# Kernel optimization log

Hardware: AMD Instinct MI355X
Metric: run time of the kernel (lower is better)

The kernel has to match this reference:

```python
import jax, jax.numpy as jnp
import numpy as np

HEADS = 16
DIM_HEAD = 64
SOFTCAP = 50.0
ROPE_THETA = 10000.0


def setup_inputs() -> dict:
    key = jax.random.key(0)
    ks = jax.random.split(key, 5)
    b, n, d, m, lmax = 2, 2048, 1024, 4, 256
    x = jax.random.normal(ks[0], (b, n, d), dtype=jnp.float32)
    tokens = jax.random.normal(ks[1], (b, m, lmax, d), dtype=jnp.float32)
    offsets = jnp.array([100, 600, 1100, 1600], dtype=jnp.int64)
    modalities = jnp.stack(
        [jnp.zeros_like(offsets), offsets, jnp.full_like(offsets, lmax)], axis=-1
    )  # [m, 3] = (type, offset, length)
    modalities = jnp.broadcast_to(modalities, (b, m, 3))
    gamma = jax.random.normal(ks[2], (d,), dtype=jnp.float32) * 0.02
    w_qkv = jax.random.normal(ks[3], (d, 3 * HEADS * DIM_HEAD), dtype=jnp.float32) / np.sqrt(d)
    w_out = jax.random.normal(ks[4], (HEADS * DIM_HEAD, d), dtype=jnp.float32) / np.sqrt(d)
    return {"x": x, "tokens": tokens, "gamma": gamma, "w_qkv": w_qkv,
            "w_out": w_out, "modalities": modalities}


def _apply_rotary(t, pos):
    # t: [b h n dh], pos: [b n] integer rotary positions (interleaved-pair rotation)
    freqs = 1.0 / (ROPE_THETA ** (jnp.arange(0, DIM_HEAD, 2, dtype=jnp.float32) / DIM_HEAD))
    ang = pos[:, None, :, None].astype(jnp.float32) * freqs  # [b 1 n dh/2]
    cos, sin = jnp.cos(ang), jnp.sin(ang)
    t1, t2 = t[..., ::2], t[..., 1::2]
    out = jnp.stack([t1 * cos - t2 * sin, t1 * sin + t2 * cos], axis=-1)
    return out.reshape(t.shape)


def reference(x, tokens, gamma, w_qkv, w_out, modalities):
    b, n, d = x.shape
    lmax = tokens.shape[2]
    off = modalities[..., 1]   # [b m]
    ln = modalities[..., 2]    # [b m]
    seq = jnp.arange(n)

    # --- embed_modality_tokens: scatter modality tokens into sequence ---
    in_span = (seq[None, None, :] >= off[..., None]) & (seq[None, None, :] < (off + ln)[..., None])  # [b m n]
    is_any = in_span.any(axis=1)  # [b n]
    rel = jnp.clip(seq[None, None, :] - off[..., None], 0, lmax - 1)  # [b m n]
    gathered = jnp.take_along_axis(tokens, rel[..., None], axis=2)  # [b m n d]
    mod_embed = jnp.einsum('bmn,bmnd->bnd', in_span.astype(x.dtype), gathered)
    x = jnp.where(is_any[..., None], mod_embed, x)

    # --- derive_rotary_positions_from_modality_positions (offset=[+1,-1]) ---
    rot_span = (seq[None, None, :] >= (off + 1)[..., None]) & (seq[None, None, :] < (off + ln)[..., None])
    pos = seq[None, :] - jnp.cumsum(rot_span.any(axis=1).astype(jnp.int32), axis=-1)  # [b n]

    # --- naive_attn_mask: causal OR within-modality bidirectional ---
    causal = seq[:, None] >= seq[None, :]  # [i j]
    mod_mask = ((seq[None, None, :, None] >= off[..., None, None]) &
                (seq[None, None, None, :] < (off + ln)[..., None, None])).any(axis=1)  # [b i j]
    mask = causal[None] | mod_mask  # [b i j]

    # --- Attention ---
    scale = DIM_HEAD ** -0.5
    xn = x / jnp.clip(jnp.linalg.norm(x, axis=-1, keepdims=True), 1e-12)
    xn = xn * (d ** 0.5) * (gamma + 1.0)  # RMSNorm (l2norm * sqrt(dim) * (gamma+1))
    qkv = (xn @ w_qkv).reshape(b, n, 3, HEADS, DIM_HEAD)
    q, k, v = (jnp.transpose(qkv[:, :, i], (0, 2, 1, 3)) for i in range(3))  # [b h n dh]
    q = _apply_rotary(q, pos)
    k = _apply_rotary(k, pos)
    scores = jnp.einsum('bhid,bhjd->bhij', q, k) * scale
    scores = jnp.tanh(scores / SOFTCAP) * SOFTCAP  # softclamp
    scores = jnp.where(mask[:, None], scores, -jnp.inf)
    attn = jax.nn.softmax(scores, axis=-1)
    out = jnp.einsum('bhij,bhjd->bhid', attn, v)
    out = jnp.transpose(out, (0, 2, 1, 3)).reshape(b, n, HEADS * DIM_HEAD)
    return out @ w_out
```

## Files before the change

kernel.cpp:

```cpp
#include <hip/hip_runtime.h>
#include <stdint.h>

#define HH 16
#define DHD 64
#define BB 2
#define NN 2048
#define DD 1024
#define MMOD 4
#define LMAX 256
#define BNROWS (BB*NN)
#define QKVN (3*HH*DHD)

typedef __attribute__((ext_vector_type(4))) float f32x4;
typedef __attribute__((ext_vector_type(8))) short s16x8;
typedef __attribute__((ext_vector_type(4))) short s16x4;

__device__ __forceinline__ float bf2f(unsigned short b) {
  return __uint_as_float(((unsigned int)b) << 16);
}
__device__ __forceinline__ unsigned short f2bf(float f) {
  unsigned int u = __float_as_uint(f);
  u += 0x7fffu + ((u >> 16) & 1u);
  return (unsigned short)(u >> 16);
}
__device__ __forceinline__ unsigned int cvt_pk_bf16(float a, float b) {
  unsigned int r;
  asm("v_cvt_pk_bf16_f32 %0, %1, %2" : "=v"(r) : "v"(a), "v"(b));
  return r;
}

#define ASYNC_LDS16(g, l) \
  __builtin_amdgcn_global_load_lds((const __attribute__((address_space(1))) void*)(g), \
                                   (__attribute__((address_space(3))) void*)(l), 16, 0, 0)

__global__ __launch_bounds__(256) void k_prep(const float* __restrict__ x,
                                              const float* __restrict__ tokens,
                                              const float* __restrict__ gamma,
                                              const int* __restrict__ mods,
                                              unsigned short* __restrict__ xn) {
  int bs = blockIdx.x;
  int bb = bs / NN, s = bs % NN;
  int t = threadIdx.x;
  int c = t * 4;
  const float4 xv = *(const float4*)(x + (size_t)bs * DD + c);
  float4 acc = {0.f, 0.f, 0.f, 0.f};
  bool any = false;
  #pragma unroll
  for (int m = 0; m < MMOD; ++m) {
    int off = mods[(bb * MMOD + m) * 3 + 1];
    int ln  = mods[(bb * MMOD + m) * 3 + 2];
    if (s >= off && s < off + ln) {
      any = true;
      int rel = s - off;
      if (rel > LMAX - 1) rel = LMAX - 1;
      if (rel < 0) rel = 0;
      const float4 tv = *(const float4*)(tokens + ((size_t)(bb * MMOD + m) * LMAX + rel) * DD + c);
      acc.x += tv.x; acc.y += tv.y; acc.z += tv.z; acc.w += tv.w;
    }
  }
  float4 v = any ? acc : xv;
  float ss = v.x*v.x + v.y*v.y + v.z*v.z + v.w*v.w;
  #pragma unroll
  for (int o = 32; o; o >>= 1) ss += __shfl_xor(ss, o);
  __shared__ float red[4];
  int wv = t >> 6;
  if ((t & 63) == 0) red[wv] = ss;
  __syncthreads();
  float tot = red[0] + red[1] + red[2] + red[3];
  float norm = sqrtf(tot);
  norm = fmaxf(norm, 1e-12f);
  float sc = 32.0f / norm;
  const float4 g = *(const float4*)(gamma + c);
  unsigned long long pk =
      (unsigned long long)f2bf(v.x * sc * (g.x + 1.f)) |
      ((unsigned long long)f2bf(v.y * sc * (g.y + 1.f)) << 16) |
      ((unsigned long long)f2bf(v.z * sc * (g.z + 1.f)) << 32) |
      ((unsigned long long)f2bf(v.w * sc * (g.w + 1.f)) << 48);
  *(unsigned long long*)(xn + (size_t)bs * DD + c) = pk;
}

__global__ void k_pos(const int* __restrict__ mods, int* __restrict__ pos) {
  int bb = blockIdx.x;
  int lane = threadIdx.x;
  int offs[MMOD], ends[MMOD];
  #pragma unroll
  for (int m = 0; m < MMOD; ++m) {
    int off = mods[(bb * MMOD + m) * 3 + 1];
    int ln  = mods[(bb * MMOD + m) * 3 + 2];
    offs[m] = off + 1;
    ends[m] = off + ln;
  }
  int base = lane * (NN / 64);
  int lc[NN / 64];
  int tot = 0;
  #pragma unroll
  for (int i = 0; i < NN / 64; ++i) {
    int s = base + i;
    int f = 0;
    #pragma unroll
    for (int m = 0; m < MMOD; ++m)
      if (s >= offs[m] && s < ends[m]) f = 1;
    tot += f;
    lc[i] = tot;
  }
  int v = tot;
  #pragma unroll
  for (int o = 1; o < 64; o <<= 1) {
    int u = __shfl_up(v, o);
    if (lane >= o) v += u;
  }
  int excl = v - tot;
  #pragma unroll
  for (int i = 0; i < NN / 64; ++i)
    pos[bb * NN + base + i] = base + i - (excl + lc[i]);
}

__global__ void k_tab(const int* __restrict__ pos, float2* __restrict__ tab) {
  int gid = blockIdx.x * 256 + threadIdx.x;
  int p = gid & 31;
  int bs = gid >> 5;
  float inv = expf(-((float)p / 32.f) * 9.210340371976184f);
  float ang = (float)pos[bs] * inv;
  float sn, cs;
  sincosf(ang, &sn, &cs);
  tab[gid] = make_float2(cs, sn);
}

__global__ void k_tr(const float* __restrict__ in, unsigned short* __restrict__ out,
                     int R, int C) {
  __shared__ float tile[32][33];
  int bx = blockIdx.x, by = blockIdx.y;
  int tx = threadIdx.x, ty = threadIdx.y;
  #pragma unroll
  for (int k = 0; k < 4; ++k) {
    int r = by * 32 + ty + k * 8, c = bx * 32 + tx;
    tile[ty + k * 8][tx] = in[(size_t)r * C + c];
  }
  __syncthreads();
  #pragma unroll
  for (int k = 0; k < 4; ++k) {
    int oc = bx * 32 + ty + k * 8;
    int orr = by * 32 + tx;
    out[(size_t)oc * R + orr] = f2bf(tile[tx][ty + k * 8]);
  }
}

template<bool F32OUT>
__global__ __launch_bounds__(256) void k_gemm(const unsigned short* __restrict__ A,
                                              const unsigned short* __restrict__ Bt,
                                              void* __restrict__ Cp,
                                              int M, int Nn, int K) {
  __shared__ unsigned short As[2][128 * 64];
  __shared__ unsigned short Bs[2][128 * 64];
  int tid = threadIdx.x;
  int lane = tid & 63, wv = tid >> 6;
  int lo = lane & 15, hi = lane >> 4;
  int nb = gridDim.x * gridDim.y;
  int fid = blockIdx.y * gridDim.x + blockIdx.x;
  int cpx = nb >> 3;
  int nid = (fid & 7) * cpx + (fid >> 3);
  int m0 = (nid / gridDim.x) * 128;
  int n0 = (nid % gridDim.x) * 128;
  int wr = wv >> 1, wc = wv & 1;
  f32x4 acc[4][4] = {};

  int srow = tid >> 3;
  int scs  = ((tid & 7) ^ ((tid >> 3) & 7)) * 8;
  #define STAGE_G(BUF, KT) do { \
    _Pragma("unroll") \
    for (int is_ = 0; is_ < 4; ++is_) { \
      int r_ = is_ * 32 + srow; \
      const unsigned short* ga_ = A  + (size_t)(m0 + r_) * K + (KT) + scs; \
      const unsigned short* gb_ = Bt + (size_t)(n0 + r_) * K + (KT) + scs; \
      ASYNC_LDS16(ga_, &As[BUF][(is_ * 256 + wv * 64) * 8]); \
      ASYNC_LDS16(gb_, &Bs[BUF][(is_ * 256 + wv * 64) * 8]); \
    } \
  } while (0)

  int nt = K >> 6;
  STAGE_G(0, 0);
  __syncthreads();
  int buf = 0;
  for (int t = 0; t < nt; ++t) {
    if (t + 1 < nt) STAGE_G(buf ^ 1, (t + 1) << 6);
    #pragma unroll
    for (int ks = 0; ks < 2; ++ks) {
      s16x8 af[4], bfr[4];
      #pragma unroll
      for (int m = 0; m < 4; ++m) {
        int row = wr * 64 + m * 16 + lo;
        int cc = ((ks * 4 + hi) ^ (lo & 7)) * 8;
        af[m] = *(const s16x8*)&As[buf][row * 64 + cc];
      }
      #pragma unroll
      for (int nn = 0; nn < 4; ++nn) {
        int row = wc * 64 + nn * 16 + lo;
        int cc = ((ks * 4 + hi) ^ (lo & 7)) * 8;
        bfr[nn] = *(const s16x8*)&Bs[buf][row * 64 + cc];
      }
      #pragma unroll
      for (int m = 0; m < 4; ++m)
        #pragma unroll
        for (int nn = 0; nn < 4; ++nn)
          acc[m][nn] = __builtin_amdgcn_mfma_f32_16x16x32_bf16(af[m], bfr[nn], acc[m][nn], 0, 0, 0);
    }
    __syncthreads();
    buf ^= 1;
  }
  #undef STAGE_G

  #pragma unroll
  for (int m = 0; m < 4; ++m) {
    #pragma unroll
    for (int nn = 0; nn < 4; ++nn) {
      int r0 = m0 + wr * 64 + m * 16 + hi * 4;
      int cc = n0 + wc * 64 + nn * 16 + lo;
      #pragma unroll
      for (int j = 0; j < 4; ++j) {
        float val = acc[m][nn][j];
        if (F32OUT) ((float*)Cp)[(size_t)(r0 + j) * Nn + cc] = val;
        else        ((unsigned short*)Cp)[(size_t)(r0 + j) * Nn + cc] = f2bf(val);
      }
    }
  }
}

__global__ __launch_bounds__(256) void k_gemm_n64(const unsigned short* __restrict__ A,
                                                  const unsigned short* __restrict__ Bt,
                                                  float* __restrict__ C,
                                                  int M, int Nn, int K) {
  __shared__ unsigned short As[2][128 * 64];
  __shared__ unsigned short Bs[2][64 * 64];
  int tid = threadIdx.x;
  int lane = tid & 63, wv = tid >> 6;
  int lo = lane & 15, hi = lane >> 4;
  int nb = gridDim.x * gridDim.y;
  int fid = blockIdx.y * gridDim.x + blockIdx.x;
  int cpx = nb >> 3;
  int nid = (fid & 7) * cpx + (fid >> 3);
  int m0 = (nid / gridDim.x) * 128;
  int n0 = (nid % gridDim.x) * 64;
  f32x4 acc[2][4] = {};

  int srow = tid >> 3;
  int scs  = ((tid & 7) ^ ((tid >> 3) & 7)) * 8;
  #define STAGE_N(BUF, KT) do { \
    _Pragma("unroll") \
    for (int is_ = 0; is_ < 4; ++is_) { \
      int r_ = is_ * 32 + srow; \
      const unsigned short* ga_ = A + (size_t)(m0 + r_) * K + (KT) + scs; \
      ASYNC_LDS16(ga_, &As[BUF][(is_ * 256 + wv * 64) * 8]); \
    } \
    _Pragma("unroll") \
    for (int is_ = 0; is_ < 2; ++is_) { \
      int r_ = is_ * 32 + srow; \
      const unsigned short* gb_ = Bt + (size_t)(n0 + r_) * K + (KT) + scs; \
      ASYNC_LDS16(gb_, &Bs[BUF][(is_ * 256 + wv * 64) * 8]); \
    } \
  } while (0)

  int nt = K >> 6;
  STAGE_N(0, 0);
  __syncthreads();
  int buf = 0;
  for (int t = 0; t < nt; ++t) {
    if (t + 1 < nt) STAGE_N(buf ^ 1, (t + 1) << 6);
    #pragma unroll
    for (int ks = 0; ks < 2; ++ks) {
      s16x8 af[2], bfr[4];
      #pragma unroll
      for (int m = 0; m < 2; ++m) {
        int row = wv * 32 + m * 16 + lo;
        int cc = ((ks * 4 + hi) ^ (lo & 7)) * 8;
        af[m] = *(const s16x8*)&As[buf][row * 64 + cc];
      }
      #pragma unroll
      for (int nn = 0; nn < 4; ++nn) {
        int row = nn * 16 + lo;
        int cc = ((ks * 4 + hi) ^ (lo & 7)) * 8;
        bfr[nn] = *(const s16x8*)&Bs[buf][row * 64 + cc];
      }
      #pragma unroll
      for (int m = 0; m < 2; ++m)
        #pragma unroll
        for (int nn = 0; nn < 4; ++nn)
          acc[m][nn] = __builtin_amdgcn_mfma_f32_16x16x32_bf16(af[m], bfr[nn], acc[m][nn], 0, 0, 0);
    }
    __syncthreads();
    buf ^= 1;
  }
  #undef STAGE_N

  #pragma unroll
  for (int m = 0; m < 2; ++m)
    #pragma unroll
    for (int nn = 0; nn < 4; ++nn) {
      int r0 = m0 + wv * 32 + m * 16 + hi * 4;
      int cc = n0 + nn * 16 + lo;
      #pragma unroll
      for (int j = 0; j < 4; ++j)
        C[(size_t)(r0 + j) * Nn + cc] = acc[m][nn][j];
    }
}

__global__ __launch_bounds__(256) void k_rope(const unsigned short* __restrict__ qkv,
                                              const float2* __restrict__ tab,
                                              unsigned short* __restrict__ k) {
  int bs = blockIdx.x;
  int bb = bs / NN, s = bs % NN;
  int lane = threadIdx.x & 63, wv = threadIdx.x >> 6;
  #pragma unroll
  for (int g = 16 + wv; g < 32; g += 4) {
    int h = g & 15;
    float val = bf2f(qkv[(size_t)bs * QKVN + g * 64 + lane]);
    float partner = __shfl_xor(val, 1);
    float2 cs = tab[(size_t)bs * 32 + (lane >> 1)];
    float out;
    if ((lane & 1) == 0) out = val * cs.x - partner * cs.y;
    else                 out = partner * cs.y + val * cs.x;
    k[((size_t)(bb * HH + h) * NN + s) * 64 + lane] = f2bf(out);
  }
}

__global__ __launch_bounds__(256) void k_vtr(const unsigned short* __restrict__ qkvt,
                                             unsigned short* __restrict__ vT) {
  __shared__ unsigned short t[64][72];
  int s0 = blockIdx.x * 64, bh = blockIdx.y, bb = bh >> 4, h = bh & 15;
  int tid = threadIdx.x;
  int r = tid >> 2, c0 = (tid & 3) * 16;
  int cw = c0 ^ (((r >> 4) & 3) << 4);
  const unsigned short* src = qkvt + (size_t)(bb * NN + s0 + r) * QKVN + 2048 + h * 64 + c0;
  *(s16x8*)&t[r][cw]     = *(const s16x8*)src;
  *(s16x8*)&t[r][cw + 8] = *(const s16x8*)(src + 8);
  __syncthreads();
  int dh = tid >> 2, sc = (tid & 3) * 16;
  int col2 = dh ^ ((tid & 3) << 4);
  s16x8 o1, o2;
  #pragma unroll
  for (int i = 0; i < 8; ++i) {
    o1[i] = (short)t[sc + i][col2];
    o2[i] = (short)t[sc + 8 + i][col2];
  }
  unsigned short* dst = vT + ((size_t)bh * 64 + dh) * NN + s0;
  int pb = (sc & 32) + (((sc >> 4) & 1) << 2);
  s16x4 g0 = __builtin_shufflevector(o1, o1, 0, 1, 2, 3);
  s16x4 g1 = __builtin_shufflevector(o1, o1, 4, 5, 6, 7);
  s16x4 g2 = __builtin_shufflevector(o2, o2, 0, 1, 2, 3);
  s16x4 g3 = __builtin_shufflevector(o2, o2, 4, 5, 6, 7);
  *(s16x4*)&dst[pb]      = g0;
  *(s16x4*)&dst[pb + 8]  = g1;
  *(s16x4*)&dst[pb + 16] = g2;
  *(s16x4*)&dst[pb + 24] = g3;
}

__global__ __launch_bounds__(512) void k_attn(const unsigned short* __restrict__ qkvt,
                                              const float2* __restrict__ tab,
                                              const unsigned short* __restrict__ k,
                                              const unsigned short* __restrict__ vT,
                                              const int* __restrict__ mods,
                                              unsigned short* __restrict__ o) {
  __shared__ unsigned short Ks[2][64 * 64];
  __shared__ unsigned short Vs[2][64 * 64];
  int tid = threadIdx.x;
  int lane = tid & 63, wv = tid >> 6;
  int lo = lane & 15, hi = lane >> 4;

  int fid = blockIdx.y * gridDim.x + blockIdx.x;
  int nid = (fid & 7) * 64 + (fid >> 3);
  int bh = nid >> 4;
  int bx = nid & 15;
  int bb = bh >> 4;
  int h = bh & 15;
  int q0A = (31 - bx) * 64;
  int q0B = bx * 64;
  int q0w = ((wv < 4) ? q0A : q0B) + (wv & 3) * 16;

  const unsigned short* kb = k + (size_t)bh * NN * 64;
  const unsigned short* vb = vT + (size_t)bh * 64 * NN;

  s16x8 qf[2];
  {
    int qrow = q0w + lo;
    const unsigned short* qp = qkvt + (size_t)(bb * NN + qrow) * QKVN + h * 64;
    const float2* tb = tab + (size_t)(bb * NN + qrow) * 32;
    #pragma unroll
    for (int ks = 0; ks < 2; ++ks) {
      s16x8 raw = *(const s16x8*)&qp[ks * 32 + hi * 8];
      #pragma unroll
      for (int e2 = 0; e2 < 4; ++e2) {
        float2 cs = tb[ks * 16 + hi * 4 + e2];
        float t1 = bf2f((unsigned short)raw[2 * e2]);
        float t2 = bf2f((unsigned short)raw[2 * e2 + 1]);
        float o1 = (t1 * cs.x - t2 * cs.y) * 0.18033688011112042f;
        float o2 = (t1 * cs.y + t2 * cs.x) * 0.18033688011112042f;
        qf[ks][2 * e2]     = (short)f2bf(o1);
        qf[ks][2 * e2 + 1] = (short)f2bf(o2);
      }
    }
  }

  int off_[MMOD], end_[MMOD];
  #pragma unroll
  for (int m = 0; m < MMOD; ++m) {
    off_[m] = mods[(bb * MMOD + m) * 3 + 1];
    end_[m] = off_[m] + mods[(bb * MMOD + m) * 3 + 2];
  }
  int limit_l;
  {
    int r = q0w + lo;
    int L = r + 1;
    #pragma unroll
    for (int m = 0; m < MMOD; ++m)
      if (off_[m] <= r && end_[m] > L) L = end_[m];
    limit_l = L;
  }
  int minlim, kvmax_w;
  {
    int L = q0w + 1;
    #pragma unroll
    for (int m = 0; m < MMOD; ++m)
      if (off_[m] <= q0w && end_[m] > L) L = end_[m];
    minlim = L;
    int r = q0w + 15;
    int L2 = r + 1;
    #pragma unroll
    for (int m = 0; m < MMOD; ++m)
      if (off_[m] <= r && end_[m] > L2) L2 = end_[m];
    kvmax_w = L2;
  }
  int nt;
  {
    int ra = q0A + 63;
    int LA = ra + 1;
    #pragma unroll
    for (int m = 0; m < MMOD; ++m)
      if (off_[m] <= ra && end_[m] > LA) LA = end_[m];
    int rb2 = q0B + 63;
    int LB = rb2 + 1;
    #pragma unroll
    for (int m = 0; m < MMOD; ++m)
      if (off_[m] <= rb2 && end_[m] > LB) LB = end_[m];
    int Lblk = (LA > LB) ? LA : LB;
    nt = (Lblk + 63) >> 6;
  }

  #define STAGE_KV(B, KV0) do { \
    int r_ = tid >> 3; \
    int cs_ = (lane & 7) ^ ((lane >> 3) & 7); \
    const unsigned short* gK_ = kb + (size_t)((KV0) + r_) * 64 + cs_ * 8; \
    ASYNC_LDS16(gK_, &Ks[B][wv * 512]); \
    const unsigned short* gV_ = vb + (size_t)r_ * NN + (KV0) + cs_ * 8; \
    ASYNC_LDS16(gV_, &Vs[B][wv * 512]); \
  } while (0)

  float lr = 0.f;
  f32x4 accO[4] = {};

  STAGE_KV(0, 0);
  __syncthreads();
  int buf = 0;
  for (int t = 0; t < nt; ++t) {
    if (t + 1 < nt) STAGE_KV(buf ^ 1, (t + 1) << 6);
    int kv0 = t << 6;
    if (kv0 < kvmax_w) {
      f32x4 sv[4];
      __builtin_amdgcn_s_setprio(1);
      #pragma unroll
      for (int cb = 0; cb < 4; ++cb) {
        int krow = cb * 16 + lo;
        int c0 = (hi) ^ (krow & 7);
        int c1 = (4 + hi) ^ (krow & 7);
        s16x8 kf0 = *(const s16x8*)&Ks[buf][krow * 64 + c0 * 8];
        s16x8 kf1 = *(const s16x8*)&Ks[buf][krow * 64 + c1 * 8];
        f32x4 z = {};
        z = __builtin_amdgcn_mfma_f32_16x16x32_bf16(kf0, qf[0], z, 0, 0, 0);
        z = __builtin_amdgcn_mfma_f32_16x16x32_bf16(kf1, qf[1], z, 0, 0, 0);
        sv[cb] = z;
      }
      __builtin_amdgcn_s_setprio(0);

      unsigned int pk_[4][2];
      bool edge = (kv0 + 64 > minlim);
      int kb0 = kv0 + hi * 4;
      #pragma unroll
      for (int cb = 0; cb < 4; ++cb) {
        float p[4];
        #pragma unroll
        for (int j = 0; j < 4; ++j) {
          float s = sv[cb][j];
          float u = __builtin_fmaf(s * s, -6.40604e-5f, 1.0f);
          float pp = __builtin_amdgcn_exp2f(s * u);
          if (edge && (kb0 + cb * 16 + j) >= limit_l) pp = 0.f;
          p[j] = pp;
        }
        lr += (p[0] + p[1]) + (p[2] + p[3]);
        pk_[cb][0] = cvt_pk_bf16(p[0], p[1]);
        pk_[cb][1] = cvt_pk_bf16(p[2], p[3]);
      }

      union { unsigned int u[4]; s16x8 v; } pa0, pa1;
      pa0.u[0] = pk_[0][0]; pa0.u[1] = pk_[0][1];
      pa0.u[2] = pk_[1][0]; pa0.u[3] = pk_[1][1];
      pa1.u[0] = pk_[2][0]; pa1.u[1] = pk_[2][1];
      pa1.u[2] = pk_[3][0]; pa1.u[3] = pk_[3][1];

      __builtin_amdgcn_s_setprio(1);
      #pragma unroll
      for (int ks = 0; ks < 2; ++ks) {
        s16x8 pa = ks ? pa1.v : pa0.v;
        #pragma unroll
        for (int cbo = 0; cbo < 4; ++cbo) {
          int vrow = cbo * 16 + lo;
          int vc = (ks * 4 + hi) ^ (vrow & 7);
          s16x8 vf = *(const s16x8*)&Vs[buf][vrow * 64 + vc * 8];
          accO[cbo] = __builtin_amdgcn_mfma_f32_16x16x32_bf16(pa, vf, accO[cbo], 0, 0, 0);
        }
      }
      __builtin_amdgcn_s_setprio(0);
    }
    __syncthreads();
    buf ^= 1;
  }

  lr += __shfl_xor(lr, 16);
  lr += __shfl_xor(lr, 32);
  float rl[4];
  #pragma unroll
  for (int j = 0; j < 4; ++j)
    rl[j] = __builtin_amdgcn_rcpf(__shfl(lr, hi * 4 + j));

  #pragma unroll
  for (int cb = 0; cb < 4; ++cb)
    #pragma unroll
    for (int j = 0; j < 4; ++j) {
      int r = q0w + hi * 4 + j;
      float val = accO[cb][j] * rl[j];
      o[((size_t)(bb * NN) + r) * (HH * DHD) + h * 64 + cb * 16 + lo] = f2bf(val);
    }
}

extern "C" void kernel_launch(void* const* d_in, const int* in_sizes, int n_in,
                              void* d_out, int out_size, void* d_ws, size_t ws_size,
                              hipStream_t stream) {
  (void)in_sizes; (void)n_in; (void)out_size; (void)ws_size;
  const float* x      = (const float*)d_in[0];
  const float* tokens = (const float*)d_in[1];
  const float* gamma  = (const float*)d_in[2];
  const float* w_qkv  = (const float*)d_in[3];
  const float* w_out  = (const float*)d_in[4];
  const int*   mods   = (const int*)d_in[5];

  char* ws = (char*)d_ws;
  unsigned short* xn    = (unsigned short*)(ws + 0);
  unsigned short* wqkvT = (unsigned short*)(ws + 8388608);
  unsigned short* woutT = (unsigned short*)(ws + 14680064);
  unsigned short* qkvt  = (unsigned short*)(ws + 16777216);
  unsigned short* kd    = (unsigned short*)(ws + 50331648);
  unsigned short* vTd   = (unsigned short*)(ws + 58720256);
  unsigned short* attno = (unsigned short*)(ws + 67108864);
  int*            pos   = (int*)(ws + 75497472);
  float2*         tab   = (float2*)(ws + 75513856);

  k_prep<<<BNROWS, 256, 0, stream>>>(x, tokens, gamma, mods, xn);
  k_pos<<<BB, 64, 0, stream>>>(mods, pos);
  k_tab<<<(BB * NN * 32) / 256, 256, 0, stream>>>(pos, tab);
  k_tr<<<dim3(QKVN / 32, DD / 32), dim3(32, 8), 0, stream>>>(w_qkv, wqkvT, DD, QKVN);
  k_tr<<<dim3((HH * DHD) / 32, DD / 32), dim3(32, 8), 0, stream>>>(w_out, woutT, HH * DHD, DD);
  k_gemm<false><<<dim3(QKVN / 128, BNROWS / 128), 256, 0, stream>>>(xn, wqkvT, (void*)qkvt, BNROWS, QKVN, DD);
  k_rope<<<BNROWS, 256, 0, stream>>>(qkvt, tab, kd);
  k_vtr<<<dim3(NN / 64, BB * HH), 256, 0, stream>>>(qkvt, vTd);
  k_attn<<<dim3(16, BB * HH), 512, 0, stream>>>(qkvt, tab, kd, vTd, mods, attno);
  k_gemm_n64<<<dim3((HH * DHD) / 64, BNROWS / 128), 256, 0, stream>>>(attno, woutT, (float*)d_out, BNROWS, DD, HH * DHD);
}
```

Measured before the change: 135.4 us.

## Switch attention to 32x32x16 MFMA with 4 waves of 32 query rows

The attention kernel moves from 16x16x32 MFMA tiles with 8 waves of 16 query rows each to 32x32x16 MFMA tiles with 4 waves of 32 rows each. The block shrinks from 512 to 256 threads, and each thread now stages two rows of K/V per tile. The V-transpose store layout and the softmax/output indexing are remapped to the 32x32 accumulator layout. Larger MFMA tiles cut LDS fragment reads per FLOP, at the cost of more accumulator registers per wave and fewer waves per block. The output GEMM is templated on output type but still writes fp32.

After: 152.9 us. 1.13x slower.

```diff
diff --git a/kernel.cpp b/kernel.cpp
--- a/kernel.cpp
+++ b/kernel.cpp
@@ -12,6 +12,7 @@
 #define QKVN (3*HH*DHD)
 
 typedef __attribute__((ext_vector_type(4))) float f32x4;
+typedef __attribute__((ext_vector_type(16))) float f32x16;
 typedef __attribute__((ext_vector_type(8))) short s16x8;
 typedef __attribute__((ext_vector_type(4))) short s16x4;
 
@@ -225,9 +226,10 @@
   }
 }
 
+template<bool F32OUT>
 __global__ __launch_bounds__(256) void k_gemm_n64(const unsigned short* __restrict__ A,
                                                   const unsigned short* __restrict__ Bt,
-                                                  float* __restrict__ C,
+                                                  void* __restrict__ Cp,
                                                   int M, int Nn, int K) {
   __shared__ unsigned short As[2][128 * 64];
   __shared__ unsigned short Bs[2][64 * 64];
@@ -298,8 +300,11 @@
       int r0 = m0 + wv * 32 + m * 16 + hi * 4;
       int cc = n0 + nn * 16 + lo;
       #pragma unroll
-      for (int j = 0; j < 4; ++j)
-        C[(size_t)(r0 + j) * Nn + cc] = acc[m][nn][j];
+      for (int j = 0; j < 4; ++j) {
+        float val = acc[m][nn][j];
+        if (F32OUT) ((float*)Cp)[(size_t)(r0 + j) * Nn + cc] = val;
+        else        ((unsigned short*)Cp)[(size_t)(r0 + j) * Nn + cc] = f2bf(val);
+      }
     }
 }
 
@@ -341,19 +346,18 @@
     o1[i] = (short)t[sc + i][col2];
     o2[i] = (short)t[sc + 8 + i][col2];
   }
-  unsigned short* dst = vT + ((size_t)bh * 64 + dh) * NN + s0;
-  int pb = (sc & 32) + (((sc >> 4) & 1) << 2);
+  unsigned short* dst = vT + ((size_t)bh * 64 + dh) * NN + s0 + sc;
   s16x4 g0 = __builtin_shufflevector(o1, o1, 0, 1, 2, 3);
   s16x4 g1 = __builtin_shufflevector(o1, o1, 4, 5, 6, 7);
   s16x4 g2 = __builtin_shufflevector(o2, o2, 0, 1, 2, 3);
   s16x4 g3 = __builtin_shufflevector(o2, o2, 4, 5, 6, 7);
-  *(s16x4*)&dst[pb]      = g0;
-  *(s16x4*)&dst[pb + 8]  = g1;
-  *(s16x4*)&dst[pb + 16] = g2;
-  *(s16x4*)&dst[pb + 24] = g3;
-}
-
-__global__ __launch_bounds__(512) void k_attn(const unsigned short* __restrict__ qkvt,
+  *(s16x4*)&dst[0]  = g0;
+  *(s16x4*)&dst[8]  = g1;
+  *(s16x4*)&dst[4]  = g2;
+  *(s16x4*)&dst[12] = g3;
+}
+
+__global__ __launch_bounds__(256) void k_attn(const unsigned short* __restrict__ qkvt,
                                               const float2* __restrict__ tab,
                                               const unsigned short* __restrict__ k,
                                               const unsigned short* __restrict__ vT,
@@ -363,7 +367,7 @@
   __shared__ unsigned short Vs[2][64 * 64];
   int tid = threadIdx.x;
   int lane = tid & 63, wv = tid >> 6;
-  int lo = lane & 15, hi = lane >> 4;
+  int l31 = lane & 31, L = lane >> 5;
 
   int fid = blockIdx.y * gridDim.x + blockIdx.x;
   int nid = (fid & 7) * 64 + (fid >> 3);
@@ -373,28 +377,28 @@
   int h = bh & 15;
   int q0A = (31 - bx) * 64;
   int q0B = bx * 64;
-  int q0w = ((wv < 4) ? q0A : q0B) + (wv & 3) * 16;
+  int q0w = ((wv < 2) ? q0A : q0B) + (wv & 1) * 32;
 
   const unsigned short* kb = k + (size_t)bh * NN * 64;
   const unsigned short* vb = vT + (size_t)bh * 64 * NN;
 
-  s16x8 qf[2];
+  s16x8 qf[4];
   {
-    int qrow = q0w + lo;
+    int qrow = q0w + l31;
     const unsigned short* qp = qkvt + (size_t)(bb * NN + qrow) * QKVN + h * 64;
     const float2* tb = tab + (size_t)(bb * NN + qrow) * 32;
     #pragma unroll
-    for (int ks = 0; ks < 2; ++ks) {
-      s16x8 raw = *(const s16x8*)&qp[ks * 32 + hi * 8];
+    for (int kc = 0; kc < 4; ++kc) {
+      s16x8 raw = *(const s16x8*)&qp[kc * 16 + L * 8];
       #pragma unroll
       for (int e2 = 0; e2 < 4; ++e2) {
-        float2 cs = tb[ks * 16 + hi * 4 + e2];
+        float2 cs = tb[kc * 8 + L * 4 + e2];
         float t1 = bf2f((unsigned short)raw[2 * e2]);
         float t2 = bf2f((unsigned short)raw[2 * e2 + 1]);
         float o1 = (t1 * cs.x - t2 * cs.y) * 0.18033688011112042f;
         float o2 = (t1 * cs.y + t2 * cs.x) * 0.18033688011112042f;
-        qf[ks][2 * e2]     = (short)f2bf(o1);
-        qf[ks][2 * e2 + 1] = (short)f2bf(o2);
+        qf[kc][2 * e2]     = (short)f2bf(o1);
+        qf[kc][2 * e2 + 1] = (short)f2bf(o2);
       }
     }
   }
@@ -407,21 +411,21 @@
   }
   int limit_l;
   {
-    int r = q0w + lo;
-    int L = r + 1;
+    int r = q0w + l31;
+    int Lm = r + 1;
     #pragma unroll
     for (int m = 0; m < MMOD; ++m)
-      if (off_[m] <= r && end_[m] > L) L = end_[m];
-    limit_l = L;
+      if (off_[m] <= r && end_[m] > Lm) Lm = end_[m];
+    limit_l = Lm;
   }
   int minlim, kvmax_w;
   {
-    int L = q0w + 1;
+    int Lm = q0w + 1;
     #pragma unroll
     for (int m = 0; m < MMOD; ++m)
-      if (off_[m] <= q0w && end_[m] > L) L = end_[m];
-    minlim = L;
-    int r = q0w + 15;
+      if (off_[m] <= q0w && end_[m] > Lm) Lm = end_[m];
+    minlim = Lm;
+    int r = q0w + 31;
     int L2 = r + 1;
     #pragma unroll
     for (int m = 0; m < MMOD; ++m)
@@ -445,16 +449,19 @@
   }
 
   #define STAGE_KV(B, KV0) do { \
-    int r_ = tid >> 3; \
-    int cs_ = (lane & 7) ^ ((lane >> 3) & 7); \
-    const unsigned short* gK_ = kb + (size_t)((KV0) + r_) * 64 + cs_ * 8; \
-    ASYNC_LDS16(gK_, &Ks[B][wv * 512]); \
-    const unsigned short* gV_ = vb + (size_t)r_ * NN + (KV0) + cs_ * 8; \
-    ASYNC_LDS16(gV_, &Vs[B][wv * 512]); \
+    _Pragma("unroll") \
+    for (int i_ = 0; i_ < 2; ++i_) { \
+      int r_ = i_ * 32 + (tid >> 3); \
+      int cs_ = (tid & 7) ^ ((tid >> 3) & 7); \
+      const unsigned short* gK_ = kb + (size_t)((KV0) + r_) * 64 + cs_ * 8; \
+      ASYNC_LDS16(gK_, &Ks[B][(i_ * 256 + wv * 64) * 8]); \
+      const unsigned short* gV_ = vb + (size_t)r_ * NN + (KV0) + cs_ * 8; \
+      ASYNC_LDS16(gV_, &Vs[B][(i_ * 256 + wv * 64) * 8]); \
+    } \
   } while (0)
 
   float lr = 0.f;
-  f32x4 accO[4] = {};
+  f32x16 accO0 = {}, accO1 = {};
 
   STAGE_KV(0, 0);
   __syncthreads();
@@ -463,58 +470,59 @@
     if (t + 1 < nt) STAGE_KV(buf ^ 1, (t + 1) << 6);
     int kv0 = t << 6;
     if (kv0 < kvmax_w) {
-      f32x4 sv[4];
+      f32x16 sv0 = {}, sv1 = {};
       __builtin_amdgcn_s_setprio(1);
       #pragma unroll
-      for (int cb = 0; cb < 4; ++cb) {
-        int krow = cb * 16 + lo;
-        int c0 = (hi) ^ (krow & 7);
-        int c1 = (4 + hi) ^ (krow & 7);
-        s16x8 kf0 = *(const s16x8*)&Ks[buf][krow * 64 + c0 * 8];
-        s16x8 kf1 = *(const s16x8*)&Ks[buf][krow * 64 + c1 * 8];
-        f32x4 z = {};
-        z = __builtin_amdgcn_mfma_f32_16x16x32_bf16(kf0, qf[0], z, 0, 0, 0);
-        z = __builtin_amdgcn_mfma_f32_16x16x32_bf16(kf1, qf[1], z, 0, 0, 0);
-        sv[cb] = z;
+      for (int kc = 0; kc < 4; ++kc) {
+        int cp = ((kc * 2 + L) ^ (lane & 7)) * 8;
+        s16x8 kf0 = *(const s16x8*)&Ks[buf][(l31) * 64 + cp];
+        s16x8 kf1 = *(const s16x8*)&Ks[buf][(32 + l31) * 64 + cp];
+        sv0 = __builtin_amdgcn_mfma_f32_32x32x16_bf16(kf0, qf[kc], sv0, 0, 0, 0);
+        sv1 = __builtin_amdgcn_mfma_f32_32x32x16_bf16(kf1, qf[kc], sv1, 0, 0, 0);
       }
       __builtin_amdgcn_s_setprio(0);
 
-      unsigned int pk_[4][2];
+      float pr0[16], pr1[16];
       bool edge = (kv0 + 64 > minlim);
-      int kb0 = kv0 + hi * 4;
-      #pragma unroll
-      for (int cb = 0; cb < 4; ++cb) {
-        float p[4];
-        #pragma unroll
-        for (int j = 0; j < 4; ++j) {
-          float s = sv[cb][j];
+      int kbase = kv0 + 4 * L;
+      #pragma unroll
+      for (int r = 0; r < 16; ++r) {
+        int koff = (r & 3) + 8 * (r >> 2);
+        {
+          float s = sv0[r];
           float u = __builtin_fmaf(s * s, -6.40604e-5f, 1.0f);
           float pp = __builtin_amdgcn_exp2f(s * u);
-          if (edge && (kb0 + cb * 16 + j) >= limit_l) pp = 0.f;
-          p[j] = pp;
+          if (edge && (kbase + koff) >= limit_l) pp = 0.f;
+          lr += pp;
+          pr0[r] = pp;
         }
-        lr += (p[0] + p[1]) + (p[2] + p[3]);
-        pk_[cb][0] = cvt_pk_bf16(p[0], p[1]);
-        pk_[cb][1] = cvt_pk_bf16(p[2], p[3]);
-      }
-
-      union { unsigned int u[4]; s16x8 v; } pa0, pa1;
-      pa0.u[0] = pk_[0][0]; pa0.u[1] = pk_[0][1];
-      pa0.u[2] = pk_[1][0]; pa0.u[3] = pk_[1][1];
-      pa1.u[0] = pk_[2][0]; pa1.u[1] = pk_[2][1];
-      pa1.u[2] = pk_[3][0]; pa1.u[3] = pk_[3][1];
+        {
+          float s = sv1[r];
+          float u = __builtin_fmaf(s * s, -6.40604e-5f, 1.0f);
+          float pp = __builtin_amdgcn_exp2f(s * u);
+          if (edge && (kbase + 32 + koff) >= limit_l) pp = 0.f;
+          lr += pp;
+          pr1[r] = pp;
+        }
+      }
+
+      union { unsigned int u[4]; s16x8 v; } pa[4];
+      #pragma unroll
+      for (int w = 0; w < 4; ++w) {
+        pa[0].u[w] = cvt_pk_bf16(pr0[2 * w],     pr0[2 * w + 1]);
+        pa[1].u[w] = cvt_pk_bf16(pr0[8 + 2 * w], pr0[8 + 2 * w + 1]);
+        pa[2].u[w] = cvt_pk_bf16(pr1[2 * w],     pr1[2 * w + 1]);
+        pa[3].u[w] = cvt_pk_bf16(pr1[8 + 2 * w], pr1[8 + 2 * w + 1]);
+      }
 
       __builtin_amdgcn_s_setprio(1);
       #pragma unroll
-      for (int ks = 0; ks < 2; ++ks) {
-        s16x8 pa = ks ? pa1.v : pa0.v;
-        #pragma unroll
-        for (int cbo = 0; cbo < 4; ++cbo) {
-          int vrow = cbo * 16 + lo;
-          int vc = (ks * 4 + hi) ^ (vrow & 7);
-          s16x8 vf = *(const s16x8*)&Vs[buf][vrow * 64 + vc * 8];
-          accO[cbo] = __builtin_amdgcn_mfma_f32_16x16x32_bf16(pa, vf, accO[cbo], 0, 0, 0);
-        }
+      for (int kc2 = 0; kc2 < 4; ++kc2) {
+        int cp = ((kc2 * 2 + L) ^ (lane & 7)) * 8;
+        s16x8 vf0 = *(const s16x8*)&Vs[buf][(l31) * 64 + cp];
+        s16x8 vf1 = *(const s16x8*)&Vs[buf][(32 + l31) * 64 + cp];
+        accO0 = __builtin_amdgcn_mfma_f32_32x32x16_bf16(pa[kc2].v, vf0, accO0, 0, 0, 0);
+        accO1 = __builtin_amdgcn_mfma_f32_32x32x16_bf16(pa[kc2].v, vf1, accO1, 0, 0, 0);
       }
       __builtin_amdgcn_s_setprio(0);
     }
@@ -522,21 +530,22 @@
     buf ^= 1;
   }
 
-  lr += __shfl_xor(lr, 16);
   lr += __shfl_xor(lr, 32);
-  float rl[4];
-  #pragma unroll
-  for (int j = 0; j < 4; ++j)
-    rl[j] = __builtin_amdgcn_rcpf(__shfl(lr, hi * 4 + j));
-
-  #pragma unroll
-  for (int cb = 0; cb < 4; ++cb)
-    #pragma unroll
-    for (int j = 0; j < 4; ++j) {
-      int r = q0w + hi * 4 + j;
-      float val = accO[cb][j] * rl[j];
-      o[((size_t)(bb * NN) + r) * (HH * DHD) + h * 64 + cb * 16 + lo] = f2bf(val);
-    }
+  float rl[16];
+  #pragma unroll
+  for (int r = 0; r < 16; ++r) {
+    int rw = (r & 3) + 8 * (r >> 2) + 4 * L;
+    rl[r] = __builtin_amdgcn_rcpf(__shfl(lr, rw));
+  }
+
+  #pragma unroll
+  for (int r = 0; r < 16; ++r) {
+    int rw = (r & 3) + 8 * (r >> 2) + 4 * L;
+    int rout = q0w + rw;
+    size_t base = ((size_t)(bb * NN) + rout) * (HH * DHD) + h * 64;
+    o[base + l31]      = f2bf(accO0[r] * rl[r]);
+    o[base + 32 + l31] = f2bf(accO1[r] * rl[r]);
+  }
 }
 
 extern "C" void kernel_launch(void* const* d_in, const int* in_sizes, int n_in,
@@ -569,6 +578,6 @@
   k_gemm<false><<<dim3(QKVN / 128, BNROWS / 128), 256, 0, stream>>>(xn, wqkvT, (void*)qkvt, BNROWS, QKVN, DD);
   k_rope<<<BNROWS, 256, 0, stream>>>(qkvt, tab, kd);
   k_vtr<<<dim3(NN / 64, BB * HH), 256, 0, stream>>>(qkvt, vTd);
-  k_attn<<<dim3(16, BB * HH), 512, 0, stream>>>(qkvt, tab, kd, vTd, mods, attno);
-  k_gemm_n64<<<dim3((HH * DHD) / 64, BNROWS / 128), 256, 0, stream>>>(attno, woutT, (float*)d_out, BNROWS, DD, HH * DHD);
-}
+  k_attn<<<dim3(16, BB * HH), 256, 0, stream>>>(qkvt, tab, kd, vTd, mods, attno);
+  k_gemm_n64<true><<<dim3(DD / 64, BNROWS / 128), 256, 0, stream>>>(attno, woutT, (void*)d_out, BNROWS, DD, HH * DHD);
+}
```
